# Optimization experiments

Measured on AMD Instinct MI355X. Metric: run time of the kernel, lower is better.

## Reference

```python
import jax, jax.numpy as jnp
import numpy as np
from jax import lax

B, T, IDIM, ODIM, L = 32, 512, 512, 80, 256
DUNITS, ATT, ACH, AK, PRE, POST = 1024, 128, 10, 31, 256, 512


def setup_inputs() -> dict:
    key = jax.random.key(0)
    ks = jax.random.split(key, 32)
    r = lambda i, shape, s=0.05: jax.random.normal(ks[i], shape, jnp.float32) * s
    d = {}
    d['hs'] = r(0, (B, T, IDIM), 1.0)
    d['hlens'] = jnp.clip(jax.random.randint(ks[1], (B,), T // 2, T + 1), 1, T)
    d['ys'] = r(2, (B, L, ODIM), 1.0)
    d['ylens'] = jnp.full((B,), L, jnp.int32)
    # location-aware attention params
    d['w_enc'] = r(3, (IDIM, ATT)); d['b_enc'] = jnp.zeros((ATT,), jnp.float32)
    d['w_dec'] = r(4, (DUNITS, ATT))
    d['loc_k'] = r(5, (ACH, 1, AK))
    d['w_loc'] = r(6, (ACH, ATT))
    d['gvec_w'] = r(7, (ATT,))
    # prenet
    d['pre_w1'] = r(8, (ODIM, PRE)); d['pre_b1'] = jnp.zeros((PRE,), jnp.float32)
    d['pre_w2'] = r(9, (PRE, PRE)); d['pre_b2'] = jnp.zeros((PRE,), jnp.float32)
    # 2 LSTM cells (torch gate order i,f,g,o; b = b_ih + b_hh)
    d['lstm0_wih'] = r(10, (4 * DUNITS, IDIM + PRE)); d['lstm0_whh'] = r(11, (4 * DUNITS, DUNITS)); d['lstm0_b'] = jnp.zeros((4 * DUNITS,), jnp.float32)
    d['lstm1_wih'] = r(12, (4 * DUNITS, DUNITS)); d['lstm1_whh'] = r(13, (4 * DUNITS, DUNITS)); d['lstm1_b'] = jnp.zeros((4 * DUNITS,), jnp.float32)
    d['feat_w'] = r(14, (DUNITS, ODIM)); d['feat_b'] = jnp.zeros((ODIM,), jnp.float32)
    d['prob_w'] = r(15, (DUNITS, 1)); d['prob_b'] = jnp.zeros((1,), jnp.float32)
    # postnet convs (no bias) + batchnorm affine
    d['post_k1'] = r(16, (POST, ODIM, 5)); d['post_k2'] = r(17, (POST, POST, 5))
    d['post_k3'] = r(18, (POST, POST, 5)); d['post_k4'] = r(19, (POST, POST, 5))
    d['post_k5'] = r(20, (ODIM, POST, 5))
    for i in range(1, 5):
        d['bn_g%d' % i] = jnp.ones((POST,), jnp.float32)
        d['bn_b%d' % i] = jnp.zeros((POST,), jnp.float32)
    return d


def _conv1d(x, k, pad):
    return lax.conv_general_dilated(x, k, (1,), [(pad, pad)], dimension_numbers=('NCH', 'OIH', 'NCH'))


def _lstm_cell(x, h, c, wih, whh, b):
    g = x @ wih.T + h @ whh.T + b
    i, f, gg, o = jnp.split(g, 4, axis=-1)
    c = jax.nn.sigmoid(f) * c + jax.nn.sigmoid(i) * jnp.tanh(gg)
    h = jax.nn.sigmoid(o) * jnp.tanh(c)
    return h, c


def _bn_train(x, g, b):
    # training-mode BatchNorm1d over (B, L) per channel; x: (B, C, L)
    m = x.mean((0, 2), keepdims=True)
    v = ((x - m) ** 2).mean((0, 2), keepdims=True)
    return g[None, :, None] * (x - m) * lax.rsqrt(v + 1e-5) + b[None, :, None]


def _forward(hs, ys, w_enc, b_enc, w_dec, loc_k, w_loc, gvec_w,
             pre_w1, pre_b1, pre_w2, pre_b2,
             lstm0_wih, lstm0_whh, lstm0_b, lstm1_wih, lstm1_whh, lstm1_b,
             feat_w, feat_b, prob_w, prob_b,
             post_k1, post_k2, post_k3, post_k4, post_k5,
             bn_g1, bn_b1, bn_g2, bn_b2, bn_g3, bn_b3, bn_g4, bn_b4, hlens):
    mask = jnp.arange(T)[None, :] < hlens[:, None]            # (B, T)
    enc_proj = hs @ w_enc + b_enc                             # (B, T, ATT)
    aw0 = mask.astype(jnp.float32) / hlens[:, None].astype(jnp.float32)
    zeros = jnp.zeros((B, DUNITS), jnp.float32)
    prev0 = jnp.broadcast_to(feat_b, (B, ODIM))               # feat_out(zero state)

    def step(carry, _):
        z0, c0, z1, c1, prev, aw = carry
        # location-aware attention
        loc = _conv1d(aw[:, None, :], loc_k, AK // 2)         # (B, ACH, T)
        e = jnp.einsum('bta,a->bt', jnp.tanh(enc_proj + (z0 @ w_dec)[:, None, :] + jnp.einsum('bct,ca->bta', loc, w_loc)), gvec_w)
        e = jnp.where(mask, e, -1e30)
        aw = jax.nn.softmax(e, axis=-1)
        att_c = jnp.einsum('bt,btd->bd', aw, hs)              # (B, IDIM)
        # prenet on previous prediction
        p = jax.nn.relu(jax.nn.relu(prev @ pre_w1 + pre_b1) @ pre_w2 + pre_b2)
        x = jnp.concatenate([att_c, p], axis=1)
        z0, c0 = _lstm_cell(x, z0, c0, lstm0_wih, lstm0_whh, lstm0_b)
        z1, c1 = _lstm_cell(z0, z1, c1, lstm1_wih, lstm1_whh, lstm1_b)
        out = z1 @ feat_w + feat_b                            # (B, ODIM)
        prob = (z1 @ prob_w + prob_b)[:, 0]                   # (B,)
        return (z0, c0, z1, c1, out, aw), (out, prob)

    _, (outs, probs) = lax.scan(step, (zeros, zeros, zeros, zeros, prev0, aw0), None, length=L)
    outs = jnp.transpose(outs, (1, 2, 0))                     # (B, ODIM, L)
    probs = probs.T                                           # (B, L)
    # postnet residual
    h = jnp.tanh(_bn_train(_conv1d(outs, post_k1, 2), bn_g1, bn_b1))
    h = jnp.tanh(_bn_train(_conv1d(h, post_k2, 2), bn_g2, bn_b2))
    h = jnp.tanh(_bn_train(_conv1d(h, post_k3, 2), bn_g3, bn_b3))
    h = jnp.tanh(_bn_train(_conv1d(h, post_k4, 2), bn_g4, bn_b4))
    h = _conv1d(h, post_k5, 2)
    outs = jnp.transpose(outs + h, (0, 2, 1))                 # (B, L, ODIM)
    return outs, probs


def reference(hs, hlens, ys, ylens, w_enc, b_enc, w_dec, loc_k, w_loc, gvec_w,
              pre_w1, pre_b1, pre_w2, pre_b2,
              lstm0_wih, lstm0_whh, lstm0_b, lstm1_wih, lstm1_whh, lstm1_b,
              feat_w, feat_b, prob_w, prob_b,
              post_k1, post_k2, post_k3, post_k4, post_k5,
              bn_g1, bn_b1, bn_g2, bn_b2, bn_g3, bn_b3, bn_g4, bn_b4):
    outs, probs = _forward(hs, ys, w_enc, b_enc, w_dec, loc_k, w_loc, gvec_w,
                           pre_w1, pre_b1, pre_w2, pre_b2,
                           lstm0_wih, lstm0_whh, lstm0_b, lstm1_wih, lstm1_whh, lstm1_b,
                           feat_w, feat_b, prob_w, prob_b,
                           post_k1, post_k2, post_k3, post_k4, post_k5,
                           bn_g1, bn_b1, bn_g2, bn_b2, bn_g3, bn_b3, bn_g4, bn_b4, hlens)
    return (outs, probs, ylens)
```

## Files before the change

kernel.cpp:

```cpp
#include <hip/hip_runtime.h>
#include <math.h>


__device__ __forceinline__ float sigm(float x){ return 1.0f/(1.0f+__expf(-x)); }


__global__ void k_init(float* __restrict__ z0, float* __restrict__ c0,
                       float* __restrict__ z1, float* __restrict__ c1,
                       float* __restrict__ aw, float* __restrict__ fw_t, float* __restrict__ wdec_t,
                       float* __restrict__ dec,
                       const float* __restrict__ feat_w, const float* __restrict__ w_dec,
                       const int* __restrict__ hlens, const int* __restrict__ ylens,
                       float* __restrict__ d_out) {
  int i = blockIdx.x*256 + threadIdx.x;
  if (i < 32768) {
    z0[i]=0.f; c0[i]=0.f; z1[i]=0.f; c1[i]=0.f;
  } else if (i < 49152) {
    int j = i - 32768; int b = j >> 9; int t = j & 511;
    int hl = hlens[b];
    aw[j] = (t < hl) ? 1.0f/(float)hl : 0.f;
  } else if (i < 131072) {
    int j = i - 49152; int od = j >> 10, k = j & 1023;
    fw_t[j] = feat_w[k*80 + od];
  } else if (i < 262144) {
    int j = i - 131072; int a = j >> 10, k = j & 1023;
    wdec_t[j] = w_dec[k*128 + a];
  } else if (i < 262176) {
    int b = i - 262144;
    d_out[663552 + b] = (float)ylens[b];
  } else if (i < 266272) {
    dec[i - 262176] = 0.f;
  }
}

__global__ void k_encproj(const float* __restrict__ hs, const float* __restrict__ w_enc,
                          const float* __restrict__ b_enc, float* __restrict__ enc_proj) {
  __shared__ float hsl[16*512];
  int b = blockIdx.x, t0 = blockIdx.y*16;
  int tid = threadIdx.x;
  for (int i = tid; i < 16*512; i += 256)
    hsl[i] = hs[(size_t)(b*512 + t0 + (i>>9))*512 + (i&511)];
  __syncthreads();
  int a = tid & 127, tq = tid >> 7;
  float acc[8];
  #pragma unroll
  for (int u=0;u<8;++u) acc[u]=0.f;
  for (int d=0; d<512; ++d) {
    float w = w_enc[d*128 + a];
    #pragma unroll
    for (int u=0;u<8;++u) acc[u] += hsl[(tq*8+u)*512 + d]*w;
  }
  float be = b_enc[a];
  #pragma unroll
  for (int u=0;u<8;++u)
    enc_proj[(size_t)(b*512 + t0 + tq*8 + u)*128 + a] = acc[u] + be;
}

__global__ __launch_bounds__(128) void k_ae(
    const float* __restrict__ z1_rd, const float* __restrict__ fw_t, const float* __restrict__ feat_b,
    const float* __restrict__ prob_w, const float* __restrict__ prob_b,
    const float* __restrict__ pre_w1, const float* __restrict__ pre_b1,
    const float* __restrict__ pre_w2, const float* __restrict__ pre_b2,
    float* __restrict__ outs_ws, float* __restrict__ probs_out, float* __restrict__ xc,
    const float* __restrict__ aw, const float* __restrict__ loc_k,
    const float* __restrict__ w_loc, const float* __restrict__ gvec,
    const float* __restrict__ enc_proj, const float* __restrict__ dec,
    const int* __restrict__ hlens, float* __restrict__ e_out,
    int store_idx, int mode) {
  int tid = threadIdx.x;
  if (blockIdx.x < 32) {
    __shared__ float zs[1024];
    __shared__ float prev[80];
    __shared__ float h1s[256];
    int b = blockIdx.x;
    for (int i = tid; i < 1024; i += 128) zs[i] = z1_rd[b*1024 + i];
    __syncthreads();
    if (tid < 80) {
      const float4* wp = (const float4*)(fw_t + tid*1024);
      float acc = feat_b[tid];
      for (int k4 = 0; k4 < 256; ++k4) {
        float4 w = wp[k4];
        acc += zs[k4*4+0]*w.x + zs[k4*4+1]*w.y + zs[k4*4+2]*w.z + zs[k4*4+3]*w.w;
      }
      prev[tid] = acc;
      if (store_idx >= 0) outs_ws[(b*80 + tid)*256 + store_idx] = acc;
    } else if (tid == 80) {
      const float4* wp = (const float4*)prob_w;
      float acc = prob_b[0];
      for (int k4 = 0; k4 < 256; ++k4) {
        float4 w = wp[k4];
        acc += zs[k4*4+0]*w.x + zs[k4*4+1]*w.y + zs[k4*4+2]*w.z + zs[k4*4+3]*w.w;
      }
      if (store_idx >= 0) probs_out[b*256 + store_idx] = acc;
    }
    if (mode == 1) return;
    __syncthreads();
    for (int j = tid; j < 256; j += 128) {
      float acc = pre_b1[j];
      for (int k = 0; k < 80; ++k) acc += prev[k]*pre_w1[k*256 + j];
      h1s[j] = fmaxf(acc, 0.f);
    }
    __syncthreads();
    for (int j = tid; j < 256; j += 128) {
      float acc = pre_b2[j];
      for (int k = 0; k < 256; ++k) acc += h1s[k]*pre_w2[k*256 + j];
      xc[b*768 + 512 + j] = fmaxf(acc, 0.f);
    }
  } else {
    int bx = blockIdx.x - 32;
    int b = bx >> 6;
    int t0 = (bx & 63)*8;
    __shared__ float awin[38];
    __shared__ float locl[10][8];
    __shared__ float red[2][8];
    if (tid < 38) {
      int idx = t0 - 15 + tid;
      awin[tid] = (idx >= 0 && idx < 512) ? aw[b*512 + idx] : 0.f;
    }
    __syncthreads();
    if (tid < 80) {
      int c = tid >> 3, tt = tid & 7;
      float s = 0.f;
      #pragma unroll
      for (int k = 0; k < 31; ++k) s += awin[tt + k]*loc_k[c*31 + k];
      locl[c][tt] = s;
    }
    __syncthreads();
    int a = tid;
    float dec_a = dec[b*128 + a];
    float gv = gvec[a];
    float wl[10];
    #pragma unroll
    for (int c = 0; c < 10; ++c) wl[c] = w_loc[c*128 + a];
    int wv = tid >> 6;
    for (int tt = 0; tt < 8; ++tt) {
      float s = enc_proj[(size_t)(b*512 + t0 + tt)*128 + a] + dec_a;
      #pragma unroll
      for (int c = 0; c < 10; ++c) s += locl[c][tt]*wl[c];
      float v = tanhf(s)*gv;
      for (int off = 32; off; off >>= 1) v += __shfl_down(v, off);
      if ((tid & 63) == 0) red[wv][tt] = v;
    }
    __syncthreads();
    if (tid < 8) {
      int t = t0 + tid;
      float ee = red[0][tid] + red[1][tid];
      int hl = hlens[b];
      e_out[b*512 + t] = (t < hl) ? ee : -1e30f;
    }
  }
}

__global__ __launch_bounds__(256) void k_attc2(const float* __restrict__ e_buf, const float* __restrict__ hs,
                                               float* __restrict__ aw_out, float* __restrict__ xc) {
  int b = blockIdx.x >> 3, dc = blockIdx.x & 7;
  int tid = threadIdx.x;
  __shared__ float aws[512];
  __shared__ float red8[8];
  __shared__ float cred[256];
  float e0 = e_buf[b*512 + tid];
  float e1 = e_buf[b*512 + 256 + tid];
  float m = fmaxf(e0, e1);
  #pragma unroll
  for (int off = 32; off; off >>= 1) m = fmaxf(m, __shfl_xor(m, off));
  if ((tid & 63) == 0) red8[tid >> 6] = m;
  __syncthreads();
  m = fmaxf(fmaxf(red8[0], red8[1]), fmaxf(red8[2], red8[3]));
  float p0 = __expf(e0 - m), p1 = __expf(e1 - m);
  float ssum = p0 + p1;
  #pragma unroll
  for (int off = 32; off; off >>= 1) ssum += __shfl_xor(ssum, off);
  if ((tid & 63) == 0) red8[4 + (tid >> 6)] = ssum;
  __syncthreads();
  float inv = 1.0f/(red8[4] + red8[5] + red8[6] + red8[7]);
  float a0 = p0*inv, a1 = p1*inv;
  aws[tid] = a0; aws[tid + 256] = a1;
  if (dc == 0) { aw_out[b*512 + tid] = a0; aw_out[b*512 + 256 + tid] = a1; }
  __syncthreads();
  int d = dc*64 + (tid & 63), w = tid >> 6;
  const float* hp  = hs + (size_t)(b*512 + w*128)*512 + d;
  const float* awp = aws + w*128;
  float acc = 0.f;
  #pragma unroll 8
  for (int t = 0; t < 128; ++t) acc += awp[t]*hp[(size_t)t*512];
  cred[w*64 + (tid & 63)] = acc;
  __syncthreads();
  if (tid < 64)
    xc[b*768 + dc*64 + tid] = cred[tid] + cred[64 + tid] + cred[128 + tid] + cred[192 + tid];
}

__global__ __launch_bounds__(256) void k_lstm2(
    const float* __restrict__ xin, int xK, const float* __restrict__ wih,
    const float* __restrict__ hin, const float* __restrict__ whh,
    const float* __restrict__ bias, float* __restrict__ cst, float* __restrict__ hnew,
    float* __restrict__ dec_out, const float* __restrict__ wdec_t) {
  __shared__ float xs[32*1028 + 4];
  int tid = threadIdx.x;

  if (blockIdx.x >= 256) {
    for (int i = tid; i < 8192; i += 256) {
      int bb = i >> 8, kq = i & 255;
      *(float4*)(xs + bb*1028 + kq*4) = *(const float4*)(xin + (size_t)bb*1024 + kq*4);
    }
    __syncthreads();
    int e4 = blockIdx.x - 256;
    int b = tid & 31, ao = tid >> 5;
    int a0 = e4*32 + ao*4;
    float s0=0.f, s1=0.f, s2=0.f, s3=0.f;
    const float4* zz = (const float4*)(xs + b*1028);
    const float4* q0 = (const float4*)(wdec_t + (size_t)(a0+0)*1024);
    const float4* q1 = (const float4*)(wdec_t + (size_t)(a0+1)*1024);
    const float4* q2 = (const float4*)(wdec_t + (size_t)(a0+2)*1024);
    const float4* q3 = (const float4*)(wdec_t + (size_t)(a0+3)*1024);
    #pragma unroll 4
    for (int k4 = 0; k4 < 256; ++k4) {
      float4 z = zz[k4];
      float4 w;
      w = q0[k4]; s0 += w.x*z.x + w.y*z.y + w.z*z.z + w.w*z.w;
      w = q1[k4]; s1 += w.x*z.x + w.y*z.y + w.z*z.z + w.w*z.w;
      w = q2[k4]; s2 += w.x*z.x + w.y*z.y + w.z*z.z + w.w*z.w;
      w = q3[k4]; s3 += w.x*z.x + w.y*z.y + w.z*z.z + w.w*z.w;
    }
    dec_out[b*128 + a0+0] = s0;
    dec_out[b*128 + a0+1] = s1;
    dec_out[b*128 + a0+2] = s2;
    dec_out[b*128 + a0+3] = s3;
    return;
  }

  int b = tid & 31, jq = tid >> 5;
  int jj0 = jq*2;
  int gate = jj0 >> 2;
  int uo0 = jj0 & 3;
  int j0 = gate*1024 + blockIdx.x*4 + uo0;
  float acc0 = bias[j0], acc1 = bias[j0 + 1];

  {
    const int S = xK + 4;
    const int qpb = xK >> 2;
    for (int i = tid; i < 32*qpb; i += 256) {
      int bb = i / qpb, kq = i - bb*qpb;
      *(float4*)(xs + bb*S + kq*4) = *(const float4*)(xin + (size_t)bb*xK + kq*4);
    }
    __syncthreads();
    const float* w0 = wih + (size_t)j0*xK;
    const float* w1 = w0 + xK;
    const float* xrow = xs + b*S;
    #pragma unroll 8
    for (int kk = 0; kk < xK; kk += 4) {
      float4 a0 = *(const float4*)(w0 + kk);
      float4 a1 = *(const float4*)(w1 + kk);
      float4 x4 = *(const float4*)(xrow + kk);
      acc0 += a0.x*x4.x + a0.y*x4.y + a0.z*x4.z + a0.w*x4.w;
      acc1 += a1.x*x4.x + a1.y*x4.y + a1.z*x4.z + a1.w*x4.w;
    }
  }
  __syncthreads();
  {
    for (int i = tid; i < 8192; i += 256) {
      int bb = i >> 8, kq = i & 255;
      *(float4*)(xs + bb*1028 + kq*4) = *(const float4*)(hin + (size_t)bb*1024 + kq*4);
    }
    __syncthreads();
    const float* v0 = whh + (size_t)j0*1024;
    const float* v1 = v0 + 1024;
    const float* xrow = xs + b*1028;
    #pragma unroll 8
    for (int kk = 0; kk < 1024; kk += 4) {
      float4 a0 = *(const float4*)(v0 + kk);
      float4 a1 = *(const float4*)(v1 + kk);
      float4 x4 = *(const float4*)(xrow + kk);
      acc0 += a0.x*x4.x + a0.y*x4.y + a0.z*x4.z + a0.w*x4.w;
      acc1 += a1.x*x4.x + a1.y*x4.y + a1.z*x4.z + a1.w*x4.w;
    }
  }
  __syncthreads();
  float* gbuf = xs;
  gbuf[jj0*33 + b] = acc0;
  gbuf[(jj0+1)*33 + b] = acc1;
  __syncthreads();
  if (tid < 128) {
    int b2 = tid & 31, uo = tid >> 5;
    float gi = gbuf[(0*4 + uo)*33 + b2];
    float gf = gbuf[(1*4 + uo)*33 + b2];
    float gg = gbuf[(2*4 + uo)*33 + b2];
    float go = gbuf[(3*4 + uo)*33 + b2];
    int u = blockIdx.x*4 + uo;
    float c_old = cst[b2*1024 + u];
    float c_new = sigm(gf)*c_old + sigm(gi)*tanhf(gg);
    float h = sigm(go)*tanhf(c_new);
    cst[b2*1024 + u] = c_new;
    hnew[b2*1024 + u] = h;
  }
}

__global__ void k_conv(const float* __restrict__ in, const float* __restrict__ wk,
                       int CI, int CO, float* __restrict__ out,
                       const float* __restrict__ resid, float* __restrict__ final_out) {
  int b = blockIdx.x, coT = blockIdx.y, lT = blockIdx.z;
  int l0 = lT*64;
  int tid = threadIdx.x;
  int lq = tid & 15, coq = tid >> 4;
  __shared__ float xs[16*68];
  __shared__ float wt[64*81];
  float acc[4][4];
  #pragma unroll
  for (int m = 0; m < 4; ++m)
    #pragma unroll
    for (int li = 0; li < 4; ++li) acc[m][li] = 0.f;
  int coBase = coT*64 + coq*4;
  for (int cc0 = 0; cc0 < CI; cc0 += 16) {
    __syncthreads();
    for (int i = tid; i < 16*68; i += 256) {
      int ci = i/68, pos = i - ci*68;
      int gl = l0 - 2 + pos;
      xs[i] = (gl >= 0 && gl < 256) ? in[((size_t)b*CI + cc0 + ci)*256 + gl] : 0.f;
    }
    for (int i = tid; i < 64*80; i += 256) {
      int co_i = i/80, rem = i - co_i*80;
      int cog = coT*64 + co_i;
      float w = (cog < CO) ? wk[(size_t)cog*CI*5 + (size_t)cc0*5 + rem] : 0.f;
      wt[co_i*81 + rem] = w;
    }
    __syncthreads();
    #pragma unroll 2
    for (int ci = 0; ci < 16; ++ci) {
      float4 xa = *(const float4*)&xs[ci*68 + lq*4];
      float4 xb = *(const float4*)&xs[ci*68 + lq*4 + 4];
      float x8[8] = {xa.x, xa.y, xa.z, xa.w, xb.x, xb.y, xb.z, xb.w};
      #pragma unroll
      for (int kk = 0; kk < 5; ++kk) {
        float w0 = wt[(coq*4+0)*81 + ci*5 + kk];
        float w1 = wt[(coq*4+1)*81 + ci*5 + kk];
        float w2 = wt[(coq*4+2)*81 + ci*5 + kk];
        float w3 = wt[(coq*4+3)*81 + ci*5 + kk];
        #pragma unroll
        for (int li = 0; li < 4; ++li) {
          float xv = x8[kk + li];
          acc[0][li] += w0*xv; acc[1][li] += w1*xv;
          acc[2][li] += w2*xv; acc[3][li] += w3*xv;
        }
      }
    }
  }
  if (final_out) {
    #pragma unroll
    for (int m = 0; m < 4; ++m) {
      int co = coBase + m;
      if (co < CO) {
        #pragma unroll
        for (int li = 0; li < 4; ++li) {
          int l = l0 + lq*4 + li;
          final_out[(size_t)(b*256 + l)*80 + co] =
              acc[m][li] + resid[((size_t)b*80 + co)*256 + l];
        }
      }
    }
  } else {
    #pragma unroll
    for (int m = 0; m < 4; ++m) {
      int co = coBase + m;
      if (co < CO) {
        float4 v = {acc[m][0], acc[m][1], acc[m][2], acc[m][3]};
        *(float4*)&out[((size_t)b*CO + co)*256 + l0 + lq*4] = v;
      }
    }
  }
}

__global__ void k_bnstats(const float* __restrict__ x, const float* __restrict__ g,
                          const float* __restrict__ bt, float* __restrict__ scale,
                          float* __restrict__ shift) {
  int c = blockIdx.x;
  int tid = threadIdx.x;
  float s = 0.f, s2 = 0.f;
  for (int i = tid; i < 8192; i += 256) {
    int bb = i >> 8, l = i & 255;
    float v = x[((size_t)bb*512 + c)*256 + l];
    s += v; s2 += v*v;
  }
  __shared__ float rs[256], rs2[256];
  rs[tid] = s; rs2[tid] = s2;
  __syncthreads();
  for (int st = 128; st; st >>= 1) {
    if (tid < st) { rs[tid] += rs[tid + st]; rs2[tid] += rs2[tid + st]; }
    __syncthreads();
  }
  if (tid == 0) {
    float m = rs[0]/8192.f;
    float var = rs2[0]/8192.f - m*m;
    float inv = rsqrtf(var + 1e-5f);
    float sc = g[c]*inv;
    scale[c] = sc;
    shift[c] = bt[c] - m*sc;
  }
}

__global__ void k_bnapply(float* __restrict__ x, const float* __restrict__ scale,
                          const float* __restrict__ shift) {
  int i = blockIdx.x*256 + threadIdx.x;
  if (i < 32*512*256) {
    int c = (i >> 8) & 511;
    x[i] = tanhf(scale[c]*x[i] + shift[c]);
  }
}

extern "C" void kernel_launch(void* const* d_in, const int* in_sizes, int n_in,
                              void* d_out, int out_size, void* d_ws, size_t ws_size,
                              hipStream_t stream) {
  const float* hs       = (const float*)d_in[0];
  const int*   hlens    = (const int*)d_in[1];
  const int*   ylens    = (const int*)d_in[3];
  const float* w_enc    = (const float*)d_in[4];
  const float* b_enc    = (const float*)d_in[5];
  const float* w_dec    = (const float*)d_in[6];
  const float* loc_k    = (const float*)d_in[7];
  const float* w_loc    = (const float*)d_in[8];
  const float* gvec     = (const float*)d_in[9];
  const float* pre_w1   = (const float*)d_in[10];
  const float* pre_b1   = (const float*)d_in[11];
  const float* pre_w2   = (const float*)d_in[12];
  const float* pre_b2   = (const float*)d_in[13];
  const float* l0_wih   = (const float*)d_in[14];
  const float* l0_whh   = (const float*)d_in[15];
  const float* l0_b     = (const float*)d_in[16];
  const float* l1_wih   = (const float*)d_in[17];
  const float* l1_whh   = (const float*)d_in[18];
  const float* l1_b     = (const float*)d_in[19];
  const float* feat_w   = (const float*)d_in[20];
  const float* feat_b   = (const float*)d_in[21];
  const float* prob_w   = (const float*)d_in[22];
  const float* prob_b   = (const float*)d_in[23];
  const float* post_k1  = (const float*)d_in[24];
  const float* post_k2  = (const float*)d_in[25];
  const float* post_k3  = (const float*)d_in[26];
  const float* post_k4  = (const float*)d_in[27];
  const float* post_k5  = (const float*)d_in[28];
  const float* bn_g1 = (const float*)d_in[29]; const float* bn_b1 = (const float*)d_in[30];
  const float* bn_g2 = (const float*)d_in[31]; const float* bn_b2 = (const float*)d_in[32];
  const float* bn_g3 = (const float*)d_in[33]; const float* bn_b3 = (const float*)d_in[34];
  const float* bn_g4 = (const float*)d_in[35]; const float* bn_b4 = (const float*)d_in[36];

  float* ws = (float*)d_ws;
  float* enc_proj = ws + 0;
  float* aw       = ws + 2097152;
  float* e        = ws + 2113536;
  float* dec      = ws + 2129920;
  float* xc       = ws + 2134016;
  float* z0       = ws + 2158592;
  float* z1       = ws + 2224128;
  float* c0       = ws + 2289664;
  float* c1       = ws + 2322432;
  float* fw_t     = ws + 2355200;
  float* wdec_t   = ws + 2437120;
  float* outs_ws  = ws + 2568192;
  float* pn1      = ws + 3223552;
  float* pn2      = ws + 7417856;
  float* bsc      = ws + 11612160;
  float* bsh      = ws + 11612672;

  float* outp  = (float*)d_out;
  float* probp = outp + 655360;

  k_init<<<1041, 256, 0, stream>>>(z0, c0, z1, c1, aw, fw_t, wdec_t, dec,
                                   feat_w, w_dec, hlens, ylens, outp);
  k_encproj<<<dim3(32, 32), 256, 0, stream>>>(hs, w_enc, b_enc, enc_proj);

  for (int s = 0; s < 256; ++s) {
    int p = s & 1;
    float* z0r = z0 + p*32768;  float* z0w = z0 + (1-p)*32768;
    float* z1r = z1 + p*32768;  float* z1w = z1 + (1-p)*32768;
    k_ae<<<2080, 128, 0, stream>>>(z1r, fw_t, feat_b, prob_w, prob_b,
                                   pre_w1, pre_b1, pre_w2, pre_b2,
                                   outs_ws, probp, xc,
                                   aw, loc_k, w_loc, gvec, enc_proj, dec, hlens, e,
                                   s - 1, 0);
    k_attc2<<<256, 256, 0, stream>>>(e, hs, aw, xc);
    k_lstm2<<<256, 256, 0, stream>>>(xc, 768, l0_wih, z0r, l0_whh, l0_b, c0, z0w,
                                     nullptr, nullptr);
    k_lstm2<<<260, 256, 0, stream>>>(z0w, 1024, l1_wih, z1r, l1_whh, l1_b, c1, z1w,
                                     dec, wdec_t);
  }
  k_ae<<<32, 128, 0, stream>>>(z1, fw_t, feat_b, prob_w, prob_b,
                               pre_w1, pre_b1, pre_w2, pre_b2,
                               outs_ws, probp, xc,
                               aw, loc_k, w_loc, gvec, enc_proj, dec, hlens, e,
                               255, 1);

  k_conv<<<dim3(32, 8, 4), 256, 0, stream>>>(outs_ws, post_k1, 80, 512, pn1, nullptr, nullptr);
  k_bnstats<<<512, 256, 0, stream>>>(pn1, bn_g1, bn_b1, bsc, bsh);
  k_bnapply<<<16384, 256, 0, stream>>>(pn1, bsc, bsh);

  k_conv<<<dim3(32, 8, 4), 256, 0, stream>>>(pn1, post_k2, 512, 512, pn2, nullptr, nullptr);
  k_bnstats<<<512, 256, 0, stream>>>(pn2, bn_g2, bn_b2, bsc, bsh);
  k_bnapply<<<16384, 256, 0, stream>>>(pn2, bsc, bsh);

  k_conv<<<dim3(32, 8, 4), 256, 0, stream>>>(pn2, post_k3, 512, 512, pn1, nullptr, nullptr);
  k_bnstats<<<512, 256, 0, stream>>>(pn1, bn_g3, bn_b3, bsc, bsh);
  k_bnapply<<<16384, 256, 0, stream>>>(pn1, bsc, bsh);

  k_conv<<<dim3(32, 8, 4), 256, 0, stream>>>(pn1, post_k4, 512, 512, pn2, nullptr, nullptr);
  k_bnstats<<<512, 256, 0, stream>>>(pn2, bn_g4, bn_b4, bsc, bsh);
  k_bnapply<<<16384, 256, 0, stream>>>(pn2, bsc, bsh);

  k_conv<<<dim3(32, 2, 4), 256, 0, stream>>>(pn2, post_k5, 512, 80, pn1, outs_ws, outp);
}
```

Baseline: 62.36 ms.

## Restructure decoder step into three fused kernels overlapping attention energies with LSTM1

Each decoder step drops from four launches to three. Softmax/context runs alongside the feature/prenet projection. LSTM0 now also emits the attention decoder projection, accumulated atomically into eight zeroed partial slices. LSTM1 runs in the same grid as the next step's location-aware energy computation. The LSTM gemv stages inputs through 256-column shared-memory chunks instead of the full row, which shrinks shared memory per block. The aim is less launch and serialization overhead on the 256-step critical path, at the cost of atomics and extra partial-sum reads.

```diff
diff --git a/kernel.cpp b/kernel.cpp
--- a/kernel.cpp
+++ b/kernel.cpp
@@ -8,10 +8,9 @@
 __global__ void k_init(float* __restrict__ z0, float* __restrict__ c0,
                        float* __restrict__ z1, float* __restrict__ c1,
                        float* __restrict__ aw, float* __restrict__ fw_t, float* __restrict__ wdec_t,
-                       float* __restrict__ dec,
                        const float* __restrict__ feat_w, const float* __restrict__ w_dec,
                        const int* __restrict__ hlens, const int* __restrict__ ylens,
-                       float* __restrict__ d_out) {
+                       float* __restrict__ d_out, float* __restrict__ dec_part) {
   int i = blockIdx.x*256 + threadIdx.x;
   if (i < 32768) {
     z0[i]=0.f; c0[i]=0.f; z1[i]=0.f; c1[i]=0.f;
@@ -28,8 +27,8 @@
   } else if (i < 262176) {
     int b = i - 262144;
     d_out[663552 + b] = (float)ylens[b];
-  } else if (i < 266272) {
-    dec[i - 262176] = 0.f;
+  } else if (i < 294944) {
+    dec_part[i - 262176] = 0.f;
   }
 }
 
@@ -56,24 +55,133 @@
     enc_proj[(size_t)(b*512 + t0 + tq*8 + u)*128 + a] = acc[u] + be;
 }
 
-__global__ __launch_bounds__(128) void k_ae(
+__device__ __forceinline__ void lstm_body(
+    const float* __restrict__ xin, int xK, const float* __restrict__ wih,
+    const float* __restrict__ hin, const float* __restrict__ whh,
+    const float* __restrict__ bias, float* __restrict__ cst, float* __restrict__ hnew,
+    int bid, int tid, float* __restrict__ xs, float* __restrict__ hb) {
+  int b = tid & 31, jq = tid >> 5;
+  int jj0 = jq*2;
+  int gate = jj0 >> 2;
+  int uo0 = jj0 & 3;
+  int j0 = gate*1024 + bid*4 + uo0;
+  float acc0 = bias[j0], acc1 = bias[j0 + 1];
+
+  const float* w0 = wih + (size_t)j0*xK;
+  const float* w1 = w0 + xK;
+  for (int c0 = 0; c0 < xK; c0 += 256) {
+    __syncthreads();
+    for (int i = tid; i < 2048; i += 256) {
+      int bb = i >> 6, kq = i & 63;
+      *(float4*)(xs + bb*260 + kq*4) = *(const float4*)(xin + (size_t)bb*xK + c0 + kq*4);
+    }
+    __syncthreads();
+    const float* xrow = xs + b*260;
+    #pragma unroll 8
+    for (int kk = 0; kk < 256; kk += 4) {
+      float4 a0 = *(const float4*)(w0 + c0 + kk);
+      float4 a1 = *(const float4*)(w1 + c0 + kk);
+      float4 x4 = *(const float4*)(xrow + kk);
+      acc0 += a0.x*x4.x + a0.y*x4.y + a0.z*x4.z + a0.w*x4.w;
+      acc1 += a1.x*x4.x + a1.y*x4.y + a1.z*x4.z + a1.w*x4.w;
+    }
+  }
+  const float* v0 = whh + (size_t)j0*1024;
+  const float* v1 = v0 + 1024;
+  for (int c0 = 0; c0 < 1024; c0 += 256) {
+    __syncthreads();
+    for (int i = tid; i < 2048; i += 256) {
+      int bb = i >> 6, kq = i & 63;
+      *(float4*)(xs + bb*260 + kq*4) = *(const float4*)(hin + (size_t)bb*1024 + c0 + kq*4);
+    }
+    __syncthreads();
+    const float* xrow = xs + b*260;
+    #pragma unroll 8
+    for (int kk = 0; kk < 256; kk += 4) {
+      float4 a0 = *(const float4*)(v0 + c0 + kk);
+      float4 a1 = *(const float4*)(v1 + c0 + kk);
+      float4 x4 = *(const float4*)(xrow + kk);
+      acc0 += a0.x*x4.x + a0.y*x4.y + a0.z*x4.z + a0.w*x4.w;
+      acc1 += a1.x*x4.x + a1.y*x4.y + a1.z*x4.z + a1.w*x4.w;
+    }
+  }
+  __syncthreads();
+  float* gbuf = xs;
+  gbuf[jj0*33 + b] = acc0;
+  gbuf[(jj0+1)*33 + b] = acc1;
+  __syncthreads();
+  if (tid < 128) {
+    int b2 = tid & 31, uo = tid >> 5;
+    float gi = gbuf[(0*4 + uo)*33 + b2];
+    float gf = gbuf[(1*4 + uo)*33 + b2];
+    float gg = gbuf[(2*4 + uo)*33 + b2];
+    float go = gbuf[(3*4 + uo)*33 + b2];
+    int u = bid*4 + uo;
+    float c_old = cst[b2*1024 + u];
+    float c_new = sigm(gf)*c_old + sigm(gi)*tanhf(gg);
+    float h = sigm(go)*tanhf(c_new);
+    cst[b2*1024 + u] = c_new;
+    hnew[b2*1024 + u] = h;
+    if (hb) hb[uo*32 + b2] = h;
+  }
+}
+
+__global__ __launch_bounds__(256) void k_d1(
     const float* __restrict__ z1_rd, const float* __restrict__ fw_t, const float* __restrict__ feat_b,
     const float* __restrict__ prob_w, const float* __restrict__ prob_b,
     const float* __restrict__ pre_w1, const float* __restrict__ pre_b1,
     const float* __restrict__ pre_w2, const float* __restrict__ pre_b2,
     float* __restrict__ outs_ws, float* __restrict__ probs_out, float* __restrict__ xc,
-    const float* __restrict__ aw, const float* __restrict__ loc_k,
-    const float* __restrict__ w_loc, const float* __restrict__ gvec,
-    const float* __restrict__ enc_proj, const float* __restrict__ dec,
-    const int* __restrict__ hlens, float* __restrict__ e_out,
+    const float* __restrict__ e_buf, const float* __restrict__ hs,
+    float* __restrict__ aw_out, float* __restrict__ dec_part,
     int store_idx, int mode) {
+  __shared__ float sm[8320];
   int tid = threadIdx.x;
-  if (blockIdx.x < 32) {
-    __shared__ float zs[1024];
-    __shared__ float prev[80];
-    __shared__ float h1s[256];
-    int b = blockIdx.x;
-    for (int i = tid; i < 1024; i += 128) zs[i] = z1_rd[b*1024 + i];
+  if (blockIdx.x < 256) {
+    if (mode == 1) return;
+    int b = blockIdx.x >> 3, dc = blockIdx.x & 7;
+    float* aws  = sm;
+    float* red8 = sm + 512;
+    float* cred = sm + 520;
+    float e0 = e_buf[b*512 + tid];
+    float e1 = e_buf[b*512 + 256 + tid];
+    float m = fmaxf(e0, e1);
+    #pragma unroll
+    for (int off = 32; off; off >>= 1) m = fmaxf(m, __shfl_xor(m, off));
+    if ((tid & 63) == 0) red8[tid >> 6] = m;
+    __syncthreads();
+    m = fmaxf(fmaxf(red8[0], red8[1]), fmaxf(red8[2], red8[3]));
+    float p0 = __expf(e0 - m), p1 = __expf(e1 - m);
+    float ssum = p0 + p1;
+    #pragma unroll
+    for (int off = 32; off; off >>= 1) ssum += __shfl_xor(ssum, off);
+    if ((tid & 63) == 0) red8[4 + (tid >> 6)] = ssum;
+    __syncthreads();
+    float inv = 1.0f/(red8[4] + red8[5] + red8[6] + red8[7]);
+    float a0 = p0*inv, a1 = p1*inv;
+    aws[tid] = a0; aws[tid + 256] = a1;
+    if (dc == 0) { aw_out[b*512 + tid] = a0; aw_out[b*512 + 256 + tid] = a1; }
+    __syncthreads();
+    int d = dc*64 + (tid & 63), w = tid >> 6;
+    const float* hp  = hs + (size_t)(b*512 + w*128)*512 + d;
+    const float* awp = aws + w*128;
+    float acc = 0.f;
+    #pragma unroll 8
+    for (int t = 0; t < 128; ++t) acc += awp[t]*hp[(size_t)t*512];
+    cred[w*64 + (tid & 63)] = acc;
+    __syncthreads();
+    if (tid < 64)
+      xc[b*768 + dc*64 + tid] = cred[tid] + cred[64 + tid] + cred[128 + tid] + cred[192 + tid];
+  } else {
+    int b = blockIdx.x - 256;
+    if (tid < 128) {
+      #pragma unroll
+      for (int sl = 0; sl < 8; ++sl) dec_part[sl*4096 + b*128 + tid] = 0.f;
+    }
+    float* zs   = sm;
+    float* prev = sm + 1024;
+    float* h1s  = sm + 1104;
+    for (int i = tid; i < 1024; i += 256) zs[i] = z1_rd[b*1024 + i];
     __syncthreads();
     if (tid < 80) {
       const float4* wp = (const float4*)(fw_t + tid*1024);
@@ -95,202 +203,101 @@
     }
     if (mode == 1) return;
     __syncthreads();
-    for (int j = tid; j < 256; j += 128) {
-      float acc = pre_b1[j];
-      for (int k = 0; k < 80; ++k) acc += prev[k]*pre_w1[k*256 + j];
-      h1s[j] = fmaxf(acc, 0.f);
-    }
-    __syncthreads();
-    for (int j = tid; j < 256; j += 128) {
-      float acc = pre_b2[j];
-      for (int k = 0; k < 256; ++k) acc += h1s[k]*pre_w2[k*256 + j];
-      xc[b*768 + 512 + j] = fmaxf(acc, 0.f);
-    }
-  } else {
-    int bx = blockIdx.x - 32;
-    int b = bx >> 6;
-    int t0 = (bx & 63)*8;
-    __shared__ float awin[38];
-    __shared__ float locl[10][8];
-    __shared__ float red[2][8];
-    if (tid < 38) {
-      int idx = t0 - 15 + tid;
-      awin[tid] = (idx >= 0 && idx < 512) ? aw[b*512 + idx] : 0.f;
-    }
-    __syncthreads();
-    if (tid < 80) {
-      int c = tid >> 3, tt = tid & 7;
-      float s = 0.f;
-      #pragma unroll
-      for (int k = 0; k < 31; ++k) s += awin[tt + k]*loc_k[c*31 + k];
-      locl[c][tt] = s;
-    }
-    __syncthreads();
-    int a = tid;
-    float dec_a = dec[b*128 + a];
-    float gv = gvec[a];
-    float wl[10];
-    #pragma unroll
-    for (int c = 0; c < 10; ++c) wl[c] = w_loc[c*128 + a];
-    int wv = tid >> 6;
-    for (int tt = 0; tt < 8; ++tt) {
-      float s = enc_proj[(size_t)(b*512 + t0 + tt)*128 + a] + dec_a;
-      #pragma unroll
-      for (int c = 0; c < 10; ++c) s += locl[c][tt]*wl[c];
-      float v = tanhf(s)*gv;
-      for (int off = 32; off; off >>= 1) v += __shfl_down(v, off);
-      if ((tid & 63) == 0) red[wv][tt] = v;
-    }
-    __syncthreads();
-    if (tid < 8) {
-      int t = t0 + tid;
-      float ee = red[0][tid] + red[1][tid];
-      int hl = hlens[b];
-      e_out[b*512 + t] = (t < hl) ? ee : -1e30f;
-    }
-  }
-}
-
-__global__ __launch_bounds__(256) void k_attc2(const float* __restrict__ e_buf, const float* __restrict__ hs,
-                                               float* __restrict__ aw_out, float* __restrict__ xc) {
-  int b = blockIdx.x >> 3, dc = blockIdx.x & 7;
+    {
+      float acc = pre_b1[tid];
+      for (int k = 0; k < 80; ++k) acc += prev[k]*pre_w1[k*256 + tid];
+      h1s[tid] = fmaxf(acc, 0.f);
+    }
+    __syncthreads();
+    {
+      float acc = pre_b2[tid];
+      for (int k = 0; k < 256; ++k) acc += h1s[k]*pre_w2[k*256 + tid];
+      xc[b*768 + 512 + tid] = fmaxf(acc, 0.f);
+    }
+  }
+}
+
+__global__ __launch_bounds__(256) void k_d2(
+    const float* __restrict__ xc, const float* __restrict__ wih,
+    const float* __restrict__ z0r, const float* __restrict__ whh,
+    const float* __restrict__ bias, float* __restrict__ c0, float* __restrict__ z0w,
+    const float* __restrict__ wdec_t, float* __restrict__ dec_part) {
+  __shared__ float sm[8320];
+  int tid = threadIdx.x, bid = blockIdx.x;
+  lstm_body(xc, 768, wih, z0r, whh, bias, c0, z0w, bid, tid, sm, sm + 528);
+  __syncthreads();
+  int b = tid & 31, aq = tid >> 5;
+  float h0 = sm[528 + 0*32 + b];
+  float h1 = sm[528 + 1*32 + b];
+  float h2 = sm[528 + 2*32 + b];
+  float h3 = sm[528 + 3*32 + b];
+  float* dp = dec_part + (bid & 7)*4096 + b*128;
+  #pragma unroll
+  for (int ai = 0; ai < 16; ++ai) {
+    int a = aq*16 + ai;
+    float4 w = *(const float4*)(wdec_t + (size_t)a*1024 + bid*4);
+    atomicAdd(dp + a, w.x*h0 + w.y*h1 + w.z*h2 + w.w*h3);
+  }
+}
+
+__global__ __launch_bounds__(256) void k_d3(
+    const float* __restrict__ z0w, const float* __restrict__ wih,
+    const float* __restrict__ z1r, const float* __restrict__ whh,
+    const float* __restrict__ bias, float* __restrict__ c1, float* __restrict__ z1w,
+    const float* __restrict__ aw, const float* __restrict__ loc_k,
+    const float* __restrict__ w_loc, const float* __restrict__ gvec,
+    const float* __restrict__ enc_proj, const float* __restrict__ dec_part,
+    const int* __restrict__ hlens, float* __restrict__ e_out, int mode) {
+  __shared__ float sm[8320];
   int tid = threadIdx.x;
-  __shared__ float aws[512];
-  __shared__ float red8[8];
-  __shared__ float cred[256];
-  float e0 = e_buf[b*512 + tid];
-  float e1 = e_buf[b*512 + 256 + tid];
-  float m = fmaxf(e0, e1);
-  #pragma unroll
-  for (int off = 32; off; off >>= 1) m = fmaxf(m, __shfl_xor(m, off));
-  if ((tid & 63) == 0) red8[tid >> 6] = m;
-  __syncthreads();
-  m = fmaxf(fmaxf(red8[0], red8[1]), fmaxf(red8[2], red8[3]));
-  float p0 = __expf(e0 - m), p1 = __expf(e1 - m);
-  float ssum = p0 + p1;
-  #pragma unroll
-  for (int off = 32; off; off >>= 1) ssum += __shfl_xor(ssum, off);
-  if ((tid & 63) == 0) red8[4 + (tid >> 6)] = ssum;
-  __syncthreads();
-  float inv = 1.0f/(red8[4] + red8[5] + red8[6] + red8[7]);
-  float a0 = p0*inv, a1 = p1*inv;
-  aws[tid] = a0; aws[tid + 256] = a1;
-  if (dc == 0) { aw_out[b*512 + tid] = a0; aw_out[b*512 + 256 + tid] = a1; }
-  __syncthreads();
-  int d = dc*64 + (tid & 63), w = tid >> 6;
-  const float* hp  = hs + (size_t)(b*512 + w*128)*512 + d;
-  const float* awp = aws + w*128;
-  float acc = 0.f;
-  #pragma unroll 8
-  for (int t = 0; t < 128; ++t) acc += awp[t]*hp[(size_t)t*512];
-  cred[w*64 + (tid & 63)] = acc;
-  __syncthreads();
-  if (tid < 64)
-    xc[b*768 + dc*64 + tid] = cred[tid] + cred[64 + tid] + cred[128 + tid] + cred[192 + tid];
-}
-
-__global__ __launch_bounds__(256) void k_lstm2(
-    const float* __restrict__ xin, int xK, const float* __restrict__ wih,
-    const float* __restrict__ hin, const float* __restrict__ whh,
-    const float* __restrict__ bias, float* __restrict__ cst, float* __restrict__ hnew,
-    float* __restrict__ dec_out, const float* __restrict__ wdec_t) {
-  __shared__ float xs[32*1028 + 4];
-  int tid = threadIdx.x;
-
-  if (blockIdx.x >= 256) {
-    for (int i = tid; i < 8192; i += 256) {
-      int bb = i >> 8, kq = i & 255;
-      *(float4*)(xs + bb*1028 + kq*4) = *(const float4*)(xin + (size_t)bb*1024 + kq*4);
-    }
-    __syncthreads();
-    int e4 = blockIdx.x - 256;
-    int b = tid & 31, ao = tid >> 5;
-    int a0 = e4*32 + ao*4;
-    float s0=0.f, s1=0.f, s2=0.f, s3=0.f;
-    const float4* zz = (const float4*)(xs + b*1028);
-    const float4* q0 = (const float4*)(wdec_t + (size_t)(a0+0)*1024);
-    const float4* q1 = (const float4*)(wdec_t + (size_t)(a0+1)*1024);
-    const float4* q2 = (const float4*)(wdec_t + (size_t)(a0+2)*1024);
-    const float4* q3 = (const float4*)(wdec_t + (size_t)(a0+3)*1024);
-    #pragma unroll 4
-    for (int k4 = 0; k4 < 256; ++k4) {
-      float4 z = zz[k4];
-      float4 w;
-      w = q0[k4]; s0 += w.x*z.x + w.y*z.y + w.z*z.z + w.w*z.w;
-      w = q1[k4]; s1 += w.x*z.x + w.y*z.y + w.z*z.z + w.w*z.w;
-      w = q2[k4]; s2 += w.x*z.x + w.y*z.y + w.z*z.z + w.w*z.w;
-      w = q3[k4]; s3 += w.x*z.x + w.y*z.y + w.z*z.z + w.w*z.w;
-    }
-    dec_out[b*128 + a0+0] = s0;
-    dec_out[b*128 + a0+1] = s1;
-    dec_out[b*128 + a0+2] = s2;
-    dec_out[b*128 + a0+3] = s3;
+  if (blockIdx.x < 256) {
+    if (mode == 1) return;
+    lstm_body(z0w, 1024, wih, z1r, whh, bias, c1, z1w, blockIdx.x, tid, sm, nullptr);
     return;
   }
-
-  int b = tid & 31, jq = tid >> 5;
-  int jj0 = jq*2;
-  int gate = jj0 >> 2;
-  int uo0 = jj0 & 3;
-  int j0 = gate*1024 + blockIdx.x*4 + uo0;
-  float acc0 = bias[j0], acc1 = bias[j0 + 1];
-
-  {
-    const int S = xK + 4;
-    const int qpb = xK >> 2;
-    for (int i = tid; i < 32*qpb; i += 256) {
-      int bb = i / qpb, kq = i - bb*qpb;
-      *(float4*)(xs + bb*S + kq*4) = *(const float4*)(xin + (size_t)bb*xK + kq*4);
-    }
-    __syncthreads();
-    const float* w0 = wih + (size_t)j0*xK;
-    const float* w1 = w0 + xK;
-    const float* xrow = xs + b*S;
-    #pragma unroll 8
-    for (int kk = 0; kk < xK; kk += 4) {
-      float4 a0 = *(const float4*)(w0 + kk);
-      float4 a1 = *(const float4*)(w1 + kk);
-      float4 x4 = *(const float4*)(xrow + kk);
-      acc0 += a0.x*x4.x + a0.y*x4.y + a0.z*x4.z + a0.w*x4.w;
-      acc1 += a1.x*x4.x + a1.y*x4.y + a1.z*x4.z + a1.w*x4.w;
-    }
-  }
-  __syncthreads();
-  {
-    for (int i = tid; i < 8192; i += 256) {
-      int bb = i >> 8, kq = i & 255;
-      *(float4*)(xs + bb*1028 + kq*4) = *(const float4*)(hin + (size_t)bb*1024 + kq*4);
-    }
-    __syncthreads();
-    const float* v0 = whh + (size_t)j0*1024;
-    const float* v1 = v0 + 1024;
-    const float* xrow = xs + b*1028;
-    #pragma unroll 8
-    for (int kk = 0; kk < 1024; kk += 4) {
-      float4 a0 = *(const float4*)(v0 + kk);
-      float4 a1 = *(const float4*)(v1 + kk);
-      float4 x4 = *(const float4*)(xrow + kk);
-      acc0 += a0.x*x4.x + a0.y*x4.y + a0.z*x4.z + a0.w*x4.w;
-      acc1 += a1.x*x4.x + a1.y*x4.y + a1.z*x4.z + a1.w*x4.w;
-    }
-  }
-  __syncthreads();
-  float* gbuf = xs;
-  gbuf[jj0*33 + b] = acc0;
-  gbuf[(jj0+1)*33 + b] = acc1;
-  __syncthreads();
-  if (tid < 128) {
-    int b2 = tid & 31, uo = tid >> 5;
-    float gi = gbuf[(0*4 + uo)*33 + b2];
-    float gf = gbuf[(1*4 + uo)*33 + b2];
-    float gg = gbuf[(2*4 + uo)*33 + b2];
-    float go = gbuf[(3*4 + uo)*33 + b2];
-    int u = blockIdx.x*4 + uo;
-    float c_old = cst[b2*1024 + u];
-    float c_new = sigm(gf)*c_old + sigm(gi)*tanhf(gg);
-    float h = sigm(go)*tanhf(c_new);
-    cst[b2*1024 + u] = c_new;
-    hnew[b2*1024 + u] = h;
+  int bx = blockIdx.x - 256;
+  int b = bx >> 5, t0 = (bx & 31)*16;
+  float* awin = sm;
+  float* locl = sm + 48;
+  float* red  = sm + 240;
+  if (tid < 46) {
+    int idx = t0 - 15 + tid;
+    awin[tid] = (idx >= 0 && idx < 512) ? aw[b*512 + idx] : 0.f;
+  }
+  __syncthreads();
+  if (tid < 160) {
+    int c = tid >> 4, tt = tid & 15;
+    float s = 0.f;
+    #pragma unroll
+    for (int k = 0; k < 31; ++k) s += awin[tt + k]*loc_k[c*31 + k];
+    locl[c*16 + tt] = s;
+  }
+  __syncthreads();
+  int a = tid & 127, th = tid >> 7, wv = tid >> 6;
+  float dec_a = 0.f;
+  #pragma unroll
+  for (int sl = 0; sl < 8; ++sl) dec_a += dec_part[sl*4096 + b*128 + a];
+  float gv = gvec[a];
+  float wl[10];
+  #pragma unroll
+  for (int c = 0; c < 10; ++c) wl[c] = w_loc[c*128 + a];
+  #pragma unroll
+  for (int tt = 0; tt < 8; ++tt) {
+    int tl = th*8 + tt;
+    float s = enc_proj[(size_t)(b*512 + t0 + tl)*128 + a] + dec_a;
+    #pragma unroll
+    for (int c = 0; c < 10; ++c) s += locl[c*16 + tl]*wl[c];
+    float v = tanhf(s)*gv;
+    #pragma unroll
+    for (int off = 32; off; off >>= 1) v += __shfl_down(v, off);
+    if ((tid & 63) == 0) red[wv*8 + tt] = v;
+  }
+  __syncthreads();
+  if (tid < 16) {
+    int t = t0 + tid;
+    float ee = (tid < 8) ? (red[tid] + red[8 + tid])
+                         : (red[16 + (tid - 8)] + red[24 + (tid - 8)]);
+    e_out[b*512 + t] = (t < hlens[b]) ? ee : -1e30f;
   }
 }
 
@@ -445,7 +452,6 @@
   float* enc_proj = ws + 0;
   float* aw       = ws + 2097152;
   float* e        = ws + 2113536;
-  float* dec      = ws + 2129920;
   float* xc       = ws + 2134016;
   float* z0       = ws + 2158592;
   float* z1       = ws + 2224128;
@@ -458,34 +464,34 @@
   float* pn2      = ws + 7417856;
   float* bsc      = ws + 11612160;
   float* bsh      = ws + 11612672;
+  float* dec_part = pn2;
 
   float* outp  = (float*)d_out;
   float* probp = outp + 655360;
 
-  k_init<<<1041, 256, 0, stream>>>(z0, c0, z1, c1, aw, fw_t, wdec_t, dec,
-                                   feat_w, w_dec, hlens, ylens, outp);
+  k_init<<<1153, 256, 0, stream>>>(z0, c0, z1, c1, aw, fw_t, wdec_t,
+                                   feat_w, w_dec, hlens, ylens, outp, dec_part);
   k_encproj<<<dim3(32, 32), 256, 0, stream>>>(hs, w_enc, b_enc, enc_proj);
+  k_d3<<<1280, 256, 0, stream>>>(z0, l1_wih, z1, l1_whh, l1_b, c1, z1,
+                                 aw, loc_k, w_loc, gvec, enc_proj, dec_part, hlens, e, 1);
 
   for (int s = 0; s < 256; ++s) {
     int p = s & 1;
     float* z0r = z0 + p*32768;  float* z0w = z0 + (1-p)*32768;
     float* z1r = z1 + p*32768;  float* z1w = z1 + (1-p)*32768;
-    k_ae<<<2080, 128, 0, stream>>>(z1r, fw_t, feat_b, prob_w, prob_b,
-                                   pre_w1, pre_b1, pre_w2, pre_b2,
-                                   outs_ws, probp, xc,
-                                   aw, loc_k, w_loc, gvec, enc_proj, dec, hlens, e,
-                                   s - 1, 0);
-    k_attc2<<<256, 256, 0, stream>>>(e, hs, aw, xc);
-    k_lstm2<<<256, 256, 0, stream>>>(xc, 768, l0_wih, z0r, l0_whh, l0_b, c0, z0w,
-                                     nullptr, nullptr);
-    k_lstm2<<<260, 256, 0, stream>>>(z0w, 1024, l1_wih, z1r, l1_whh, l1_b, c1, z1w,
-                                     dec, wdec_t);
-  }
-  k_ae<<<32, 128, 0, stream>>>(z1, fw_t, feat_b, prob_w, prob_b,
-                               pre_w1, pre_b1, pre_w2, pre_b2,
-                               outs_ws, probp, xc,
-                               aw, loc_k, w_loc, gvec, enc_proj, dec, hlens, e,
-                               255, 1);
+    k_d1<<<288, 256, 0, stream>>>(z1r, fw_t, feat_b, prob_w, prob_b,
+                                  pre_w1, pre_b1, pre_w2, pre_b2,
+                                  outs_ws, probp, xc, e, hs, aw, dec_part,
+                                  s - 1, 0);
+    k_d2<<<256, 256, 0, stream>>>(xc, l0_wih, z0r, l0_whh, l0_b, c0, z0w,
+                                  wdec_t, dec_part);
+    k_d3<<<1280, 256, 0, stream>>>(z0w, l1_wih, z1r, l1_whh, l1_b, c1, z1w,
+                                   aw, loc_k, w_loc, gvec, enc_proj, dec_part, hlens, e, 0);
+  }
+  k_d1<<<288, 256, 0, stream>>>(z1, fw_t, feat_b, prob_w, prob_b,
+                                pre_w1, pre_b1, pre_w2, pre_b2,
+                                outs_ws, probp, xc, e, hs, aw, dec_part,
+                                255, 1);
 
   k_conv<<<dim3(32, 8, 4), 256, 0, stream>>>(outs_ws, post_k1, 80, 512, pn1, nullptr, nullptr);
   k_bnstats<<<512, 256, 0, stream>>>(pn1, bn_g1, bn_b1, bsc, bsh);
```

New measurement: 56.13 ms. 10.0% less time.
